# Optimization experiments

Measured on AMD Instinct MI355X. Metric: run time of the kernel, lower is better.

## Reference

```python
import jax, jax.numpy as jnp
import numpy as np

B, T, H, K = 64, 1024, 256, 4  # batch, seq_len, hidden_dim, crf_size


def setup_inputs() -> dict:
    key = jax.random.key(0)
    ks = jax.random.split(key, 8)
    return {
        "sentence_features": jax.random.normal(ks[0], (B, T, H), dtype=jnp.float32),
        "conv_w": jax.random.normal(ks[1], (H, H, 3), dtype=jnp.float32) * (1.0 / np.sqrt(3 * H)),
        "conv_b": jnp.zeros((H,), dtype=jnp.float32),
        "lin_w": jax.random.normal(ks[2], (K, H), dtype=jnp.float32) * (1.0 / np.sqrt(H)),
        "lin_b": jnp.zeros((K,), dtype=jnp.float32),
        "crf_start": jax.random.uniform(ks[3], (K,), dtype=jnp.float32, minval=-0.1, maxval=0.1),
        "crf_end": jax.random.uniform(ks[4], (K,), dtype=jnp.float32, minval=-0.1, maxval=0.1),
        "crf_trans": jax.random.uniform(ks[5], (K, K), dtype=jnp.float32, minval=-0.1, maxval=0.1),
    }


def _emissions(x, conv_w, conv_b, lin_w, lin_b):
    # x: [B, T, H] -> transpose -> Conv1d(k=3, pad=1) -> ReLU -> transpose -> Linear
    xc = jnp.swapaxes(x, 1, 2)  # [B, H, T]
    y = jax.lax.conv_general_dilated(
        xc, conv_w, window_strides=(1,), padding=((1, 1),),
        dimension_numbers=("NCH", "OIH", "NCH"))
    y = jax.nn.relu(y + conv_b[None, :, None])
    y = jnp.swapaxes(y, 1, 2)  # [B, T, H]
    return y @ lin_w.T + lin_b  # [B, T, K]


def _viterbi_decode(em, start, end, trans):
    # em: [B, T, K]; torchcrf CRF.decode with no mask (batch_first=True)
    score0 = start[None, :] + em[:, 0]  # [B, K]

    def step(score, emit_t):
        # score [B, K] over prev tag; broadcast to [B, K_prev, K_next]
        nxt = score[:, :, None] + trans[None, :, :] + emit_t[:, None, :]
        return jnp.max(nxt, axis=1), jnp.argmax(nxt, axis=1)  # new score, best prev tag

    em_rest = jnp.swapaxes(em[:, 1:], 0, 1)  # [T-1, B, K]
    final, history = jax.lax.scan(step, score0, em_rest)
    final = final + end[None, :]
    last_tag = jnp.argmax(final, axis=-1)  # [B]

    def back(tag, idx_t):
        prev = jnp.take_along_axis(idx_t, tag[:, None], axis=1)[:, 0]
        return prev, prev

    _, tags_head = jax.lax.scan(back, last_tag, history, reverse=True)  # [T-1, B]
    path = jnp.concatenate([jnp.swapaxes(tags_head, 0, 1), last_tag[:, None]], axis=1)
    return path.astype(jnp.int32)  # [B, T]


def reference(sentence_features, conv_w, conv_b, lin_w, lin_b, crf_start, crf_end, crf_trans):
    em = _emissions(sentence_features, conv_w, conv_b, lin_w, lin_b)
    return _viterbi_decode(em, crf_start, crf_end, crf_trans)
```

## Files before the change

### kernel.cpp

```cpp
#include <hip/hip_runtime.h>
#include <cstdint>
#include <cstddef>

typedef __attribute__((ext_vector_type(8))) short short8;
typedef __attribute__((ext_vector_type(4))) float f32x4;

constexpr int Bn = 64, Tn = 1024, Hn = 256, Kn = 4;
constexpr int TT = 128;
constexpr int AROWS = TT + 2;
constexpr int ARSTR = 144;
constexpr int ABUFSZ = AROWS * ARSTR;

__device__ __forceinline__ unsigned bf16rne(float f) {
  unsigned u = __float_as_uint(f);
  return (u + 0x7fffu + ((u >> 16) & 1u)) >> 16;
}

__global__ __launch_bounds__(256) void pack_b_k(const float* __restrict__ conv_w,
                                                unsigned short* __restrict__ Bp) {
  int gt = blockIdx.x * 256 + threadIdx.x;
  int fid = gt >> 6, l = gt & 63;
  int ks = fid >> 5, rem = fid & 31;
  int p = rem >> 4, nf = rem & 15;
  int n = nf * 16 + (l & 15);
  int k0 = ks * 32 + ((l >> 4) << 3);
  short8 s;
  #pragma unroll
  for (int j = 0; j < 8; ++j) {
    int k = k0 + j;
    int dt = k >> 8, i = k & 255;
    float w = conv_w[n * 768 + i * 3 + dt];
    unsigned hb = bf16rne(w);
    if (p == 0) s[j] = (short)hb;
    else        s[j] = (short)bf16rne(w - __uint_as_float(hb << 16));
  }
  *reinterpret_cast<short8*>(Bp + (size_t)fid * 512 + l * 8) = s;
}

#define GBAR() asm volatile("s_waitcnt lgkmcnt(0)\n\ts_barrier" ::: "memory")

__global__ __launch_bounds__(256, 2) void emis_k(const float* __restrict__ x,
    const unsigned short* __restrict__ Bp, const float* __restrict__ conv_b,
    const float* __restrict__ lin_w, float* __restrict__ em2) {
  __shared__ __align__(16) char A_lds[2 * ABUFSZ];

  const int b = blockIdx.z, ny = blockIdx.y, t0 = blockIdx.x * TT;
  const int tid = threadIdx.x, lane = tid & 63, w = tid >> 6;
  const int wm = w >> 1, wn = w & 1;
  const float* xb = x + (size_t)b * Tn * Hn;

  float4 pre[5];

  auto loadA = [&](int ig) {
    #pragma unroll
    for (int it = 0; it < 5; ++it) {
      int idx = it * 256 + tid;
      if (idx < AROWS * 8) {
        int row = idx >> 3, c4 = idx & 7;
        int trow = t0 - 1 + row;
        float4 v = make_float4(0.f, 0.f, 0.f, 0.f);
        if (trow >= 0 && trow < Tn)
          v = *reinterpret_cast<const float4*>(xb + (size_t)trow * Hn + ig * 32 + c4 * 4);
        pre[it] = v;
      }
    }
  };
  auto writeA = [&](int boff) {
    #pragma unroll
    for (int it = 0; it < 5; ++it) {
      int idx = it * 256 + tid;
      if (idx < AROWS * 8) {
        int row = idx >> 3, c4 = idx & 7;
        float vf[4] = {pre[it].x, pre[it].y, pre[it].z, pre[it].w};
        unsigned h[4], lo[4];
        #pragma unroll
        for (int q = 0; q < 4; ++q) {
          h[q] = bf16rne(vf[q]);
          lo[q] = bf16rne(vf[q] - __uint_as_float(h[q] << 16));
        }
        uint2 hp, lp;
        hp.x = h[0] | (h[1] << 16);  hp.y = h[2] | (h[3] << 16);
        lp.x = lo[0] | (lo[1] << 16); lp.y = lo[2] | (lo[3] << 16);
        char* base = A_lds + boff + row * ARSTR + c4 * 8;
        *reinterpret_cast<uint2*>(base) = hp;
        *reinterpret_cast<uint2*>(base + 64) = lp;
      }
    }
  };

  const char* bsrc = reinterpret_cast<const char*>(Bp)
      + (size_t)(ny * 8 + wn * 4) * 1024 + lane * 16;
  auto loadB = [&](short8* Bh, short8* Bl, int ks) {
    #pragma unroll
    for (int nf = 0; nf < 4; ++nf) {
      Bh[nf] = *reinterpret_cast<const short8*>(bsrc + (size_t)((ks * 2 + 0) * 16 + nf) * 1024);
      Bl[nf] = *reinterpret_cast<const short8*>(bsrc + (size_t)((ks * 2 + 1) * 16 + nf) * 1024);
    }
  };

  f32x4 acc[4][4];
  #pragma unroll
  for (int mf = 0; mf < 4; ++mf)
    #pragma unroll
    for (int nf = 0; nf < 4; ++nf) acc[mf][nf] = (f32x4)0.f;

  const char* aB = A_lds + (lane & 15) * ARSTR + ((lane >> 4) << 4) + wm * 64 * ARSTR;

#define STEP(ABUF, DT, BH, BL, NBH, NBL, KSN)                                 \
  {                                                                           \
    loadB(NBH, NBL, (KSN));                                                   \
    __builtin_amdgcn_s_setprio(1);                                            \
    _Pragma("unroll")                                                         \
    for (int mf = 0; mf < 4; ++mf) {                                          \
      const char* ap = aB + (ABUF) + (mf * 16 + (DT)) * ARSTR;                \
      short8 Ah = *reinterpret_cast<const short8*>(ap);                       \
      short8 Al = *reinterpret_cast<const short8*>(ap + 64);                  \
      _Pragma("unroll")                                                       \
      for (int nf = 0; nf < 4; ++nf) {                                        \
        f32x4 c = acc[mf][nf];                                                \
        c = __builtin_amdgcn_mfma_f32_16x16x32_bf16(Ah, BH[nf], c, 0, 0, 0);  \
        c = __builtin_amdgcn_mfma_f32_16x16x32_bf16(Al, BH[nf], c, 0, 0, 0);  \
        c = __builtin_amdgcn_mfma_f32_16x16x32_bf16(Ah, BL[nf], c, 0, 0, 0);  \
        acc[mf][nf] = c;                                                      \
      }                                                                       \
    }                                                                         \
    __builtin_amdgcn_s_setprio(0);                                            \
  }

  short8 BhA[4], BlA[4], BhB[4], BlB[4];
  loadA(0);
  loadB(BhA, BlA, 0);
  writeA(0);
  GBAR();

  #pragma unroll 1
  for (int igp = 0; igp < 4; ++igp) {
    const int ig0 = igp * 2, ig1 = ig0 + 1;
    loadA(ig1);
    STEP(0, 0, BhA, BlA, BhB, BlB, 8 + ig0);
    STEP(0, 1, BhB, BlB, BhA, BlA, 16 + ig0);
    STEP(0, 2, BhA, BlA, BhB, BlB, ig1);
    writeA(ABUFSZ);
    GBAR();
    if (ig1 < 7) loadA(ig1 + 1);
    STEP(ABUFSZ, 0, BhB, BlB, BhA, BlA, 8 + ig1);
    STEP(ABUFSZ, 1, BhA, BlA, BhB, BlB, 16 + ig1);
    STEP(ABUFSZ, 2, BhB, BlB, BhA, BlA, (ig1 < 7 ? ig1 + 1 : 0));
    if (ig1 < 7) writeA(0);
    GBAR();
  }
#undef STEP

  f32x4 pem[4][4];
  #pragma unroll
  for (int mf = 0; mf < 4; ++mf)
    #pragma unroll
    for (int v = 0; v < 4; ++v) pem[mf][v] = (f32x4)0.f;

  #pragma unroll
  for (int nf = 0; nf < 4; ++nf) {
    const int gcol = ny * 128 + wn * 64 + nf * 16 + (lane & 15);
    const float cb = conv_b[gcol];
    f32x4 lw;
    lw[0] = lin_w[gcol]; lw[1] = lin_w[256 + gcol];
    lw[2] = lin_w[512 + gcol]; lw[3] = lin_w[768 + gcol];
    #pragma unroll
    for (int mf = 0; mf < 4; ++mf)
      #pragma unroll
      for (int v = 0; v < 4; ++v) {
        float val = fmaxf(acc[mf][nf][v] + cb, 0.f);
        pem[mf][v] += val * lw;
      }
  }
  #pragma unroll
  for (int mf = 0; mf < 4; ++mf)
    #pragma unroll
    for (int v = 0; v < 4; ++v) {
      f32x4 t = pem[mf][v];
      #pragma unroll
      for (int m = 1; m < 16; m <<= 1) {
        f32x4 q;
        q[0] = __shfl_xor(t[0], m); q[1] = __shfl_xor(t[1], m);
        q[2] = __shfl_xor(t[2], m); q[3] = __shfl_xor(t[3], m);
        t += q;
      }
      pem[mf][v] = t;
    }
  __syncthreads();
  float* red = reinterpret_cast<float*>(A_lds);
  if ((lane & 15) == 0) {
    const int g = lane >> 4;
    #pragma unroll
    for (int mf = 0; mf < 4; ++mf)
      #pragma unroll
      for (int v = 0; v < 4; ++v) {
        int r = wm * 64 + mf * 16 + g * 4 + v;
        *reinterpret_cast<f32x4*>(red + (r * 2 + wn) * 4) = pem[mf][v];
      }
  }
  __syncthreads();
  if (tid < 128) {
    f32x4 s0 = *reinterpret_cast<f32x4*>(red + tid * 8);
    f32x4 s1 = *reinterpret_cast<f32x4*>(red + tid * 8 + 4);
    f32x4 s = s0 + s1;
    *reinterpret_cast<f32x4*>(em2 + ((size_t)(b * Tn + t0 + tid) * 2 + ny) * 4) = s;
  }
}

__device__ __forceinline__ unsigned int compose_map(unsigned int a, unsigned int b) {
#if __has_builtin(__builtin_amdgcn_perm)
  return __builtin_amdgcn_perm(a, a, b);
#else
  unsigned int c = 0;
  #pragma unroll
  for (int k = 0; k < 4; ++k) {
    unsigned int sel = (b >> (8 * k)) & 0xffu;
    c |= ((a >> (8 * sel)) & 0xffu) << (8 * k);
  }
  return c;
#endif
}

template <int J>
__device__ __forceinline__ float qb(float v) {
  return __int_as_float(__builtin_amdgcn_update_dpp(
      0, __float_as_int(v), (J * 0x55), 0xf, 0xf, true));
}

#define PSTEP(EV, T)                                                       \
  {                                                                        \
    shf[((T) - 1) * 4 + kk] = s;                                           \
    float c0 = qb<0>(s) + trc0;                                            \
    float c1 = qb<1>(s) + trc1;                                            \
    float c2 = qb<2>(s) + trc2;                                            \
    float c3 = qb<3>(s) + trc3;                                            \
    s = fmaxf(fmaxf(c0, c1), fmaxf(c2, c3)) + (EV);                        \
  }

__global__ __launch_bounds__(64) void viterbi_k(const float* __restrict__ em2,
    const float* __restrict__ lin_b, const float* __restrict__ cstart,
    const float* __restrict__ cend, const float* __restrict__ ctrans,
    int* __restrict__ out) {
  __shared__ float4 se[Tn];
  __shared__ float4 sh[Tn - 1];
  __shared__ int s_last;
  const int b = blockIdx.x, lane = threadIdx.x;
  const float4* e2 = reinterpret_cast<const float4*>(em2 + (size_t)b * Tn * 8);
  const float lb0 = lin_b[0], lb1 = lin_b[1], lb2 = lin_b[2], lb3 = lin_b[3];
  for (int i = lane; i < Tn; i += 64) {
    float4 a = e2[i * 2], c = e2[i * 2 + 1];
    se[i] = make_float4(a.x + c.x + lb0, a.y + c.y + lb1,
                        a.z + c.z + lb2, a.w + c.w + lb3);
  }
  float tr[4][4];
  #pragma unroll
  for (int j = 0; j < 4; ++j)
    #pragma unroll
    for (int k = 0; k < 4; ++k) tr[j][k] = ctrans[j * 4 + k];
  __syncthreads();

  if (lane < 4) {
    const int kk = lane;
    const float* sef = reinterpret_cast<const float*>(se);
    float* shf = reinterpret_cast<float*>(sh);
    const float trc0 = ctrans[0 * 4 + kk];
    const float trc1 = ctrans[1 * 4 + kk];
    const float trc2 = ctrans[2 * 4 + kk];
    const float trc3 = ctrans[3 * 4 + kk];
    float s = cstart[kk] + sef[kk];
    float e[8];
    #pragma unroll
    for (int d = 0; d < 8; ++d) e[d] = sef[(1 + d) * 4 + kk];
    int t = 1;
    #pragma unroll 1
    for (int g = 0; g < 127; ++g, t += 8) {
      float f[8];
      #pragma unroll
      for (int d = 0; d < 8; ++d) f[d] = e[d];
      #pragma unroll
      for (int d = 0; d < 8; ++d) e[d] = sef[(t + 8 + d) * 4 + kk];
      PSTEP(f[0], t);     PSTEP(f[1], t + 1);
      PSTEP(f[2], t + 2); PSTEP(f[3], t + 3);
      PSTEP(f[4], t + 4); PSTEP(f[5], t + 5);
      PSTEP(f[6], t + 6); PSTEP(f[7], t + 7);
    }
    PSTEP(e[0], 1017); PSTEP(e[1], 1018); PSTEP(e[2], 1019);
    PSTEP(e[3], 1020); PSTEP(e[4], 1021); PSTEP(e[5], 1022);
    PSTEP(e[6], 1023);
    s += cend[kk];
    float f0 = __shfl(s, 0), f1 = __shfl(s, 1);
    float f2 = __shfl(s, 2), f3 = __shfl(s, 3);
    if (kk == 0) {
      int tag = 0; float bf = f0;
      if (f1 > bf) { bf = f1; tag = 1; }
      if (f2 > bf) { bf = f2; tag = 2; }
      if (f3 > bf) { bf = f3; tag = 3; }
      s_last = tag;
    }
  }
  __syncthreads();

  const unsigned int ID = 0x03020100u;
  unsigned int mloc[16];
  const int t0 = lane * 16;
  #pragma unroll
  for (int k = 0; k < 16; ++k) {
    const int t = t0 + k;
    if (t < Tn - 1) {
      const float4 s = sh[t];
      const float4 e = se[t + 1];
      const float sj[4] = {s.x, s.y, s.z, s.w};
      const float ev[4] = {e.x, e.y, e.z, e.w};
      unsigned int mw = 0;
      #pragma unroll
      for (int kk = 0; kk < 4; ++kk) {
        float best = (sj[0] + tr[0][kk]) + ev[kk];
        int bi = 0;
        #pragma unroll
        for (int j = 1; j < 4; ++j) {
          float cc = (sj[j] + tr[j][kk]) + ev[kk];
          if (cc > best) { best = cc; bi = j; }
        }
        mw |= (unsigned)bi << (8 * kk);
      }
      mloc[k] = mw;
    } else {
      mloc[k] = ID;
    }
  }
  unsigned int P = mloc[15];
  #pragma unroll
  for (int k = 14; k >= 0; --k) P = compose_map(mloc[k], P);
  #pragma unroll
  for (int d = 1; d < 64; d <<= 1) {
    unsigned int q = (unsigned int)__shfl_down((int)P, d);
    if (lane + d > 63) q = ID;
    P = compose_map(P, q);
  }
  unsigned int E = (unsigned int)__shfl_down((int)P, 1);
  if (lane == 63) E = ID;
  const int last = s_last;
  unsigned int tag = (E >> (8 * last)) & 3u;
  int* ob = out + (size_t)b * Tn;
  #pragma unroll
  for (int k = 15; k >= 0; --k) {
    tag = (mloc[k] >> (8 * tag)) & 3u;
    ob[t0 + k] = (int)tag;
  }
}

extern "C" void kernel_launch(void* const* d_in, const int* in_sizes, int n_in,
                              void* d_out, int out_size, void* d_ws, size_t ws_size,
                              hipStream_t stream) {
  const float* x      = (const float*)d_in[0];
  const float* conv_w = (const float*)d_in[1];
  const float* conv_b = (const float*)d_in[2];
  const float* lin_w  = (const float*)d_in[3];
  const float* lin_b  = (const float*)d_in[4];
  const float* cstart = (const float*)d_in[5];
  const float* cend   = (const float*)d_in[6];
  const float* ctrans = (const float*)d_in[7];
  int* out = (int*)d_out;

  unsigned short* Bp = (unsigned short*)d_ws;
  float* em2 = (float*)((char*)d_ws + 786432);

  pack_b_k<<<192, 256, 0, stream>>>(conv_w, Bp);
  emis_k<<<dim3(Tn / TT, 2, Bn), 256, 0, stream>>>(x, Bp, conv_b, lin_w, em2);
  viterbi_k<<<Bn, 64, 0, stream>>>(em2, lin_b, cstart, cend, ctrans, out);
}
```

Measured before the change: 123.4 us.

## Presplit x into swizzled bf16 hi/lo tiles and stage via direct global-to-LDS loads

Adds a presplit kernel that converts x once into padded, XOR-swizzled bf16 hi/lo tiles in workspace. The GEMM kernel then stages A straight into LDS with global_load_lds, so the per-block fp32-to-bf16 split and register round trip are gone. It also uses a smaller LDS stride and targets 3 blocks per SM. In exchange it adds an extra pass that writes and rereads a bf16 copy of x in global memory, and it needs a larger workspace, falling back to the old kernel if the workspace is too small.

```diff
diff --git a/kernel.cpp b/kernel.cpp
--- a/kernel.cpp
+++ b/kernel.cpp
@@ -10,6 +10,9 @@
 constexpr int AROWS = TT + 2;
 constexpr int ARSTR = 144;
 constexpr int ABUFSZ = AROWS * ARSTR;
+constexpr int ARSTR2 = 128;
+constexpr int ABUFSZ2 = AROWS * ARSTR2;
+constexpr int XROWS = Tn + 2;
 
 __device__ __forceinline__ unsigned bf16rne(float f) {
   unsigned u = __float_as_uint(f);
@@ -37,9 +40,198 @@
   *reinterpret_cast<short8*>(Bp + (size_t)fid * 512 + l * 8) = s;
 }
 
+__global__ __launch_bounds__(256) void presplit_k(const float* __restrict__ x,
+                                                  unsigned char* __restrict__ xs) {
+  int idx = blockIdx.x * 256 + threadIdx.x;
+  if (idx >= XROWS * 8) return;
+  const int bg = blockIdx.y;
+  const int kgp = idx & 7, trow1 = idx >> 3;
+  const int t = trow1 - 1;
+  const int kg = kgp ^ (trow1 & 7);
+  unsigned short o[8] = {0, 0, 0, 0, 0, 0, 0, 0};
+  if (t >= 0 && t < Tn) {
+    const int b = bg >> 3, ig = bg & 7;
+    const int c8 = ig * 32 + (kg & 3) * 8;
+    const float* src = x + ((size_t)b * Tn + t) * Hn + c8;
+    float4 v0 = *reinterpret_cast<const float4*>(src);
+    float4 v1 = *reinterpret_cast<const float4*>(src + 4);
+    float vf[8] = {v0.x, v0.y, v0.z, v0.w, v1.x, v1.y, v1.z, v1.w};
+    if (kg < 4) {
+      #pragma unroll
+      for (int j = 0; j < 8; ++j) o[j] = (unsigned short)bf16rne(vf[j]);
+    } else {
+      #pragma unroll
+      for (int j = 0; j < 8; ++j) {
+        unsigned hb = bf16rne(vf[j]);
+        o[j] = (unsigned short)bf16rne(vf[j] - __uint_as_float(hb << 16));
+      }
+    }
+  }
+  short8 s;
+  #pragma unroll
+  for (int j = 0; j < 8; ++j) s[j] = (short)o[j];
+  *reinterpret_cast<short8*>(xs + ((size_t)bg * XROWS * 8 + idx) * 16) = s;
+}
+
+__device__ __forceinline__ void gload_lds16(const void* g, void* l) {
+  __builtin_amdgcn_global_load_lds(
+      (const __attribute__((address_space(1))) void*)g,
+      (__attribute__((address_space(3))) void*)l, 16, 0, 0);
+}
+
+__global__ __launch_bounds__(256, 3) void emis_k(
+    const unsigned char* __restrict__ xs, const unsigned short* __restrict__ Bp,
+    const float* __restrict__ conv_b, const float* __restrict__ lin_w,
+    float* __restrict__ em2) {
+  __shared__ __align__(16) char A_lds[2 * ABUFSZ2];
+
+  const int b = blockIdx.z, ny = blockIdx.y, t0 = blockIdx.x * TT;
+  const int tid = threadIdx.x, lane = tid & 63, w = tid >> 6;
+  const int wm = w >> 1, wn = w & 1;
+
+  auto stageA = [&](int boff, int ig) {
+    const unsigned char* src = xs + ((size_t)(b * 8 + ig) * XROWS + t0) * 128;
+    #pragma unroll
+    for (int it = 0; it < 4; ++it) {
+      const int cbase = (w * 4 + it) * 64;
+      gload_lds16(src + (size_t)(cbase + lane) * 16,
+                  A_lds + boff + (cbase + lane) * 16);
+    }
+    if (w == 0)
+      gload_lds16(src + (size_t)(976 + lane) * 16,
+                  A_lds + boff + (976 + lane) * 16);
+  };
+
+  const char* bsrc = reinterpret_cast<const char*>(Bp)
+      + (size_t)(ny * 8 + wn * 4) * 1024 + lane * 16;
+  auto loadB = [&](short8* Bh, short8* Bl, int ks) {
+    #pragma unroll
+    for (int nf = 0; nf < 4; ++nf) {
+      Bh[nf] = *reinterpret_cast<const short8*>(bsrc + (size_t)((ks * 2 + 0) * 16 + nf) * 1024);
+      Bl[nf] = *reinterpret_cast<const short8*>(bsrc + (size_t)((ks * 2 + 1) * 16 + nf) * 1024);
+    }
+  };
+
+  f32x4 acc[4][4];
+  #pragma unroll
+  for (int mf = 0; mf < 4; ++mf)
+    #pragma unroll
+    for (int nf = 0; nf < 4; ++nf) acc[mf][nf] = (f32x4)0.f;
+
+  const int l7 = lane & 7, kh = lane >> 4;
+  const int Abase = ((lane & 15) + wm * 64) * ARSTR2;
+  const char* vAh[3];
+  const char* vAl[3];
+  #pragma unroll
+  for (int dt = 0; dt < 3; ++dt) {
+    const int s = (l7 + dt) & 7;
+    vAh[dt] = A_lds + Abase + dt * ARSTR2 + ((kh ^ s) << 4);
+    vAl[dt] = A_lds + Abase + dt * ARSTR2 + (((kh + 4) ^ s) << 4);
+  }
+
+#define BAR8() asm volatile("s_waitcnt vmcnt(8) lgkmcnt(0)\n\ts_barrier" ::: "memory")
+
+#define STEPN(ABUF, DT, BH, BL, NBH, NBL, KSN)                                \
+  {                                                                           \
+    loadB(NBH, NBL, (KSN));                                                   \
+    __builtin_amdgcn_s_setprio(1);                                            \
+    _Pragma("unroll")                                                         \
+    for (int mf = 0; mf < 4; ++mf) {                                          \
+      short8 Ah = *reinterpret_cast<const short8*>(vAh[DT] + (ABUF) + mf * 2048); \
+      short8 Al = *reinterpret_cast<const short8*>(vAl[DT] + (ABUF) + mf * 2048); \
+      _Pragma("unroll")                                                       \
+      for (int nf = 0; nf < 4; ++nf) {                                        \
+        f32x4 c = acc[mf][nf];                                                \
+        c = __builtin_amdgcn_mfma_f32_16x16x32_bf16(Ah, BH[nf], c, 0, 0, 0);  \
+        c = __builtin_amdgcn_mfma_f32_16x16x32_bf16(Al, BH[nf], c, 0, 0, 0);  \
+        c = __builtin_amdgcn_mfma_f32_16x16x32_bf16(Ah, BL[nf], c, 0, 0, 0);  \
+        acc[mf][nf] = c;                                                      \
+      }                                                                       \
+    }                                                                         \
+    __builtin_amdgcn_s_setprio(0);                                            \
+  }
+
+  short8 BhA[4], BlA[4], BhB[4], BlB[4];
+  loadB(BhA, BlA, 0);
+  stageA(0, 0);
+  asm volatile("s_waitcnt vmcnt(0) lgkmcnt(0)\n\ts_barrier" ::: "memory");
+
+  #pragma unroll 1
+  for (int igp = 0; igp < 4; ++igp) {
+    const int ig0 = igp * 2, ig1 = ig0 + 1;
+    stageA(ABUFSZ2, ig1);
+    STEPN(0, 0, BhA, BlA, BhB, BlB, 8 + ig0);
+    STEPN(0, 1, BhB, BlB, BhA, BlA, 16 + ig0);
+    STEPN(0, 2, BhA, BlA, BhB, BlB, ig1);
+    BAR8();
+    if (ig1 < 7) stageA(0, ig1 + 1);
+    STEPN(ABUFSZ2, 0, BhB, BlB, BhA, BlA, 8 + ig1);
+    STEPN(ABUFSZ2, 1, BhA, BlA, BhB, BlB, 16 + ig1);
+    STEPN(ABUFSZ2, 2, BhB, BlB, BhA, BlA, (ig1 < 7 ? ig1 + 1 : 0));
+    BAR8();
+  }
+#undef STEPN
+#undef BAR8
+
+  f32x4 pem[4][4];
+  #pragma unroll
+  for (int mf = 0; mf < 4; ++mf)
+    #pragma unroll
+    for (int v = 0; v < 4; ++v) pem[mf][v] = (f32x4)0.f;
+
+  #pragma unroll
+  for (int nf = 0; nf < 4; ++nf) {
+    const int gcol = ny * 128 + wn * 64 + nf * 16 + (lane & 15);
+    const float cb = conv_b[gcol];
+    f32x4 lw;
+    lw[0] = lin_w[gcol]; lw[1] = lin_w[256 + gcol];
+    lw[2] = lin_w[512 + gcol]; lw[3] = lin_w[768 + gcol];
+    #pragma unroll
+    for (int mf = 0; mf < 4; ++mf)
+      #pragma unroll
+      for (int v = 0; v < 4; ++v) {
+        float val = fmaxf(acc[mf][nf][v] + cb, 0.f);
+        pem[mf][v] += val * lw;
+      }
+  }
+  #pragma unroll
+  for (int mf = 0; mf < 4; ++mf)
+    #pragma unroll
+    for (int v = 0; v < 4; ++v) {
+      f32x4 t = pem[mf][v];
+      #pragma unroll
+      for (int m = 1; m < 16; m <<= 1) {
+        f32x4 q;
+        q[0] = __shfl_xor(t[0], m); q[1] = __shfl_xor(t[1], m);
+        q[2] = __shfl_xor(t[2], m); q[3] = __shfl_xor(t[3], m);
+        t += q;
+      }
+      pem[mf][v] = t;
+    }
+  __syncthreads();
+  float* red = reinterpret_cast<float*>(A_lds);
+  if ((lane & 15) == 0) {
+    const int g = lane >> 4;
+    #pragma unroll
+    for (int mf = 0; mf < 4; ++mf)
+      #pragma unroll
+      for (int v = 0; v < 4; ++v) {
+        int r = wm * 64 + mf * 16 + g * 4 + v;
+        *reinterpret_cast<f32x4*>(red + (r * 2 + wn) * 4) = pem[mf][v];
+      }
+  }
+  __syncthreads();
+  if (tid < 128) {
+    f32x4 s0 = *reinterpret_cast<f32x4*>(red + tid * 8);
+    f32x4 s1 = *reinterpret_cast<f32x4*>(red + tid * 8 + 4);
+    f32x4 s = s0 + s1;
+    *reinterpret_cast<f32x4*>(em2 + ((size_t)(b * Tn + t0 + tid) * 2 + ny) * 4) = s;
+  }
+}
+
 #define GBAR() asm volatile("s_waitcnt lgkmcnt(0)\n\ts_barrier" ::: "memory")
 
-__global__ __launch_bounds__(256, 2) void emis_k(const float* __restrict__ x,
+__global__ __launch_bounds__(256, 2) void emis_k13(const float* __restrict__ x,
     const unsigned short* __restrict__ Bp, const float* __restrict__ conv_b,
     const float* __restrict__ lin_w, float* __restrict__ em2) {
   __shared__ __align__(16) char A_lds[2 * ABUFSZ];
@@ -50,7 +242,6 @@
   const float* xb = x + (size_t)b * Tn * Hn;
 
   float4 pre[5];
-
   auto loadA = [&](int ig) {
     #pragma unroll
     for (int it = 0; it < 5; ++it) {
@@ -106,7 +297,7 @@
 
   const char* aB = A_lds + (lane & 15) * ARSTR + ((lane >> 4) << 4) + wm * 64 * ARSTR;
 
-#define STEP(ABUF, DT, BH, BL, NBH, NBL, KSN)                                 \
+#define STEP13(ABUF, DT, BH, BL, NBH, NBL, KSN)                               \
   {                                                                           \
     loadB(NBH, NBL, (KSN));                                                   \
     __builtin_amdgcn_s_setprio(1);                                            \
@@ -137,19 +328,19 @@
   for (int igp = 0; igp < 4; ++igp) {
     const int ig0 = igp * 2, ig1 = ig0 + 1;
     loadA(ig1);
-    STEP(0, 0, BhA, BlA, BhB, BlB, 8 + ig0);
-    STEP(0, 1, BhB, BlB, BhA, BlA, 16 + ig0);
-    STEP(0, 2, BhA, BlA, BhB, BlB, ig1);
+    STEP13(0, 0, BhA, BlA, BhB, BlB, 8 + ig0);
+    STEP13(0, 1, BhB, BlB, BhA, BlA, 16 + ig0);
+    STEP13(0, 2, BhA, BlA, BhB, BlB, ig1);
     writeA(ABUFSZ);
     GBAR();
     if (ig1 < 7) loadA(ig1 + 1);
-    STEP(ABUFSZ, 0, BhB, BlB, BhA, BlA, 8 + ig1);
-    STEP(ABUFSZ, 1, BhA, BlA, BhB, BlB, 16 + ig1);
-    STEP(ABUFSZ, 2, BhB, BlB, BhA, BlA, (ig1 < 7 ? ig1 + 1 : 0));
+    STEP13(ABUFSZ, 0, BhB, BlB, BhA, BlA, 8 + ig1);
+    STEP13(ABUFSZ, 1, BhA, BlA, BhB, BlB, 16 + ig1);
+    STEP13(ABUFSZ, 2, BhB, BlB, BhA, BlA, (ig1 < 7 ? ig1 + 1 : 0));
     if (ig1 < 7) writeA(0);
     GBAR();
   }
-#undef STEP
+#undef STEP13
 
   f32x4 pem[4][4];
   #pragma unroll
@@ -364,8 +555,16 @@
 
   unsigned short* Bp = (unsigned short*)d_ws;
   float* em2 = (float*)((char*)d_ws + 786432);
+  unsigned char* xs = (unsigned char*)d_ws + 786432 + 2097152;
+  const size_t xs_bytes = (size_t)Bn * 8 * XROWS * 128;
+  const size_t need = 786432 + 2097152 + xs_bytes;
 
   pack_b_k<<<192, 256, 0, stream>>>(conv_w, Bp);
-  emis_k<<<dim3(Tn / TT, 2, Bn), 256, 0, stream>>>(x, Bp, conv_b, lin_w, em2);
+  if (ws_size >= need) {
+    presplit_k<<<dim3((XROWS * 8 + 255) / 256, Bn * 8), 256, 0, stream>>>(x, xs);
+    emis_k<<<dim3(Tn / TT, 2, Bn), 256, 0, stream>>>(xs, Bp, conv_b, lin_w, em2);
+  } else {
+    emis_k13<<<dim3(Tn / TT, 2, Bn), 256, 0, stream>>>(x, Bp, conv_b, lin_w, em2);
+  }
   viterbi_k<<<Bn, 64, 0, stream>>>(em2, lin_b, cstart, cend, ctrans, out);
 }
```

Result: slower. 146.0 us (+18.3%).

## Compute all 256 output channels per block to load each input tile once

Applied to the files above, without the earlier changes.

The emission kernel now has each block cover the full 256 conv output channels for its 128-timestep tile, instead of splitting channels across two blocks. Each wave owns 64 columns and all 128 rows, so the input tile is loaded and bf16-split once rather than twice, and the cross-block partial-emission sum in the Viterbi kernel goes away. In exchange, accumulators double to 128 floats per thread, raising register pressure at two blocks per SIMD, and the grid shrinks to half as many blocks.

```diff
diff --git a/kernel.cpp b/kernel.cpp
--- a/kernel.cpp
+++ b/kernel.cpp
@@ -41,12 +41,11 @@
 
 __global__ __launch_bounds__(256, 2) void emis_k(const float* __restrict__ x,
     const unsigned short* __restrict__ Bp, const float* __restrict__ conv_b,
-    const float* __restrict__ lin_w, float* __restrict__ em2) {
+    const float* __restrict__ lin_w, float* __restrict__ em) {
   __shared__ __align__(16) char A_lds[2 * ABUFSZ];
 
-  const int b = blockIdx.z, ny = blockIdx.y, t0 = blockIdx.x * TT;
+  const int b = blockIdx.y, t0 = blockIdx.x * TT;
   const int tid = threadIdx.x, lane = tid & 63, w = tid >> 6;
-  const int wm = w >> 1, wn = w & 1;
   const float* xb = x + (size_t)b * Tn * Hn;
 
   float4 pre[5];
@@ -89,7 +88,7 @@
   };
 
   const char* bsrc = reinterpret_cast<const char*>(Bp)
-      + (size_t)(ny * 8 + wn * 4) * 1024 + lane * 16;
+      + (size_t)(w * 4) * 1024 + lane * 16;
   auto loadB = [&](short8* Bh, short8* Bl, int ks) {
     #pragma unroll
     for (int nf = 0; nf < 4; ++nf) {
@@ -98,20 +97,22 @@
     }
   };
 
-  f32x4 acc[4][4];
-  #pragma unroll
-  for (int mf = 0; mf < 4; ++mf)
+  f32x4 acc[8][4];
+  #pragma unroll
+  for (int mf = 0; mf < 8; ++mf)
     #pragma unroll
     for (int nf = 0; nf < 4; ++nf) acc[mf][nf] = (f32x4)0.f;
 
-  const char* aB = A_lds + (lane & 15) * ARSTR + ((lane >> 4) << 4) + wm * 64 * ARSTR;
+  const char* aB = A_lds + (lane & 15) * ARSTR + ((lane >> 4) << 4);
+
+  short8 BhA[4], BlA[4], BhB[4], BlB[4];
 
 #define STEP(ABUF, DT, BH, BL, NBH, NBL, KSN)                                 \
   {                                                                           \
     loadB(NBH, NBL, (KSN));                                                   \
     __builtin_amdgcn_s_setprio(1);                                            \
     _Pragma("unroll")                                                         \
-    for (int mf = 0; mf < 4; ++mf) {                                          \
+    for (int mf = 0; mf < 8; ++mf) {                                          \
       const char* ap = aB + (ABUF) + (mf * 16 + (DT)) * ARSTR;                \
       short8 Ah = *reinterpret_cast<const short8*>(ap);                       \
       short8 Al = *reinterpret_cast<const short8*>(ap + 64);                  \
@@ -127,7 +128,6 @@
     __builtin_amdgcn_s_setprio(0);                                            \
   }
 
-  short8 BhA[4], BlA[4], BhB[4], BlB[4];
   loadA(0);
   loadB(BhA, BlA, 0);
   writeA(0);
@@ -151,32 +151,29 @@
   }
 #undef STEP
 
-  f32x4 pem[4][4];
-  #pragma unroll
-  for (int mf = 0; mf < 4; ++mf)
-    #pragma unroll
-    for (int v = 0; v < 4; ++v) pem[mf][v] = (f32x4)0.f;
-
-  #pragma unroll
-  for (int nf = 0; nf < 4; ++nf) {
-    const int gcol = ny * 128 + wn * 64 + nf * 16 + (lane & 15);
-    const float cb = conv_b[gcol];
-    f32x4 lw;
-    lw[0] = lin_w[gcol]; lw[1] = lin_w[256 + gcol];
-    lw[2] = lin_w[512 + gcol]; lw[3] = lin_w[768 + gcol];
-    #pragma unroll
-    for (int mf = 0; mf < 4; ++mf)
+  __syncthreads();
+  float* red = reinterpret_cast<float*>(A_lds);
+  #pragma unroll 1
+  for (int mf = 0; mf < 8; ++mf) {
+    f32x4 pem[4];
+    #pragma unroll
+    for (int v = 0; v < 4; ++v) pem[v] = (f32x4)0.f;
+    #pragma unroll
+    for (int nf = 0; nf < 4; ++nf) {
+      const int gcol = w * 64 + nf * 16 + (lane & 15);
+      const float cb = conv_b[gcol];
+      f32x4 lw;
+      lw[0] = lin_w[gcol]; lw[1] = lin_w[256 + gcol];
+      lw[2] = lin_w[512 + gcol]; lw[3] = lin_w[768 + gcol];
       #pragma unroll
       for (int v = 0; v < 4; ++v) {
         float val = fmaxf(acc[mf][nf][v] + cb, 0.f);
-        pem[mf][v] += val * lw;
-      }
-  }
-  #pragma unroll
-  for (int mf = 0; mf < 4; ++mf)
+        pem[v] += val * lw;
+      }
+    }
     #pragma unroll
     for (int v = 0; v < 4; ++v) {
-      f32x4 t = pem[mf][v];
+      f32x4 t = pem[v];
       #pragma unroll
       for (int m = 1; m < 16; m <<= 1) {
         f32x4 q;
@@ -184,26 +181,20 @@
         q[2] = __shfl_xor(t[2], m); q[3] = __shfl_xor(t[3], m);
         t += q;
       }
-      pem[mf][v] = t;
-    }
+      if ((lane & 15) == 0) {
+        const int r = mf * 16 + (lane >> 4) * 4 + v;
+        *reinterpret_cast<f32x4*>(red + (r * 4 + w) * 4) = t;
+      }
+    }
+  }
   __syncthreads();
-  float* red = reinterpret_cast<float*>(A_lds);
-  if ((lane & 15) == 0) {
-    const int g = lane >> 4;
-    #pragma unroll
-    for (int mf = 0; mf < 4; ++mf)
-      #pragma unroll
-      for (int v = 0; v < 4; ++v) {
-        int r = wm * 64 + mf * 16 + g * 4 + v;
-        *reinterpret_cast<f32x4*>(red + (r * 2 + wn) * 4) = pem[mf][v];
-      }
-  }
-  __syncthreads();
-  if (tid < 128) {
-    f32x4 s0 = *reinterpret_cast<f32x4*>(red + tid * 8);
-    f32x4 s1 = *reinterpret_cast<f32x4*>(red + tid * 8 + 4);
-    f32x4 s = s0 + s1;
-    *reinterpret_cast<f32x4*>(em2 + ((size_t)(b * Tn + t0 + tid) * 2 + ny) * 4) = s;
+  if (tid < TT) {
+    f32x4 s0 = *reinterpret_cast<f32x4*>(red + (tid * 4 + 0) * 4);
+    f32x4 s1 = *reinterpret_cast<f32x4*>(red + (tid * 4 + 1) * 4);
+    f32x4 s2 = *reinterpret_cast<f32x4*>(red + (tid * 4 + 2) * 4);
+    f32x4 s3 = *reinterpret_cast<f32x4*>(red + (tid * 4 + 3) * 4);
+    f32x4 s = ((s0 + s1) + s2) + s3;
+    *reinterpret_cast<f32x4*>(em + (size_t)(b * Tn + t0 + tid) * 4) = s;
   }
 }
 
@@ -237,7 +228,7 @@
     s = fmaxf(fmaxf(c0, c1), fmaxf(c2, c3)) + (EV);                        \
   }
 
-__global__ __launch_bounds__(64) void viterbi_k(const float* __restrict__ em2,
+__global__ __launch_bounds__(64) void viterbi_k(const float* __restrict__ em,
     const float* __restrict__ lin_b, const float* __restrict__ cstart,
     const float* __restrict__ cend, const float* __restrict__ ctrans,
     int* __restrict__ out) {
@@ -245,12 +236,11 @@
   __shared__ float4 sh[Tn - 1];
   __shared__ int s_last;
   const int b = blockIdx.x, lane = threadIdx.x;
-  const float4* e2 = reinterpret_cast<const float4*>(em2 + (size_t)b * Tn * 8);
+  const float4* e4 = reinterpret_cast<const float4*>(em + (size_t)b * Tn * Kn);
   const float lb0 = lin_b[0], lb1 = lin_b[1], lb2 = lin_b[2], lb3 = lin_b[3];
   for (int i = lane; i < Tn; i += 64) {
-    float4 a = e2[i * 2], c = e2[i * 2 + 1];
-    se[i] = make_float4(a.x + c.x + lb0, a.y + c.y + lb1,
-                        a.z + c.z + lb2, a.w + c.w + lb3);
+    float4 a = e4[i];
+    se[i] = make_float4(a.x + lb0, a.y + lb1, a.z + lb2, a.w + lb3);
   }
   float tr[4][4];
   #pragma unroll
@@ -363,9 +353,9 @@
   int* out = (int*)d_out;
 
   unsigned short* Bp = (unsigned short*)d_ws;
-  float* em2 = (float*)((char*)d_ws + 786432);
+  float* em = (float*)((char*)d_ws + 786432);
 
   pack_b_k<<<192, 256, 0, stream>>>(conv_w, Bp);
-  emis_k<<<dim3(Tn / TT, 2, Bn), 256, 0, stream>>>(x, Bp, conv_b, lin_w, em2);
-  viterbi_k<<<Bn, 64, 0, stream>>>(em2, lin_b, cstart, cend, ctrans, out);
-}
+  emis_k<<<dim3(Tn / TT, Bn), 256, 0, stream>>>(x, Bp, conv_b, lin_w, em);
+  viterbi_k<<<Bn, 64, 0, stream>>>(em, lin_b, cstart, cend, ctrans, out);
+}
```

Measured after the change: 211.9 us. +71.7%, slower.
